# Kernel optimization log

Measured on AMD Instinct MI355X. Metric: run time of the kernel, lower is better.

Reference implementation:

```python
import jax, jax.numpy as jnp
import numpy as np

WINDOW = (2, 7, 7)
SHIFT = (1, 3, 3)
HEADS = 4


def _rel_pos_index(ws):
    coords = np.stack(np.meshgrid(*[np.arange(w) for w in ws], indexing='ij'))  # (3, wd, wh, ww)
    cf = coords.reshape(3, -1)
    rel = cf[:, :, None] - cf[:, None, :]  # (3, N, N)
    rel = rel.transpose(1, 2, 0).astype(np.int64)
    rel[:, :, 0] += ws[0] - 1
    rel[:, :, 1] += ws[1] - 1
    rel[:, :, 2] += ws[2] - 1
    rel[:, :, 0] *= (2 * ws[1] - 1) * (2 * ws[2] - 1)
    rel[:, :, 1] *= 2 * ws[2] - 1
    return rel.sum(-1)  # (N, N)


def _attn_mask(D, H, W, ws, ss):
    img = np.zeros((1, D, H, W, 1), np.float32)
    cnt = 0
    for d in (slice(None, -ws[0]), slice(-ws[0], -ss[0]), slice(-ss[0], None)):
        for h in (slice(None, -ws[1]), slice(-ws[1], -ss[1]), slice(-ss[1], None)):
            for w in (slice(None, -ws[2]), slice(-ws[2], -ss[2]), slice(-ss[2], None)):
                img[:, d, h, w, :] = cnt
                cnt += 1
    N = ws[0] * ws[1] * ws[2]
    mw = img.reshape(1, D // ws[0], ws[0], H // ws[1], ws[1], W // ws[2], ws[2], 1)
    mw = mw.transpose(0, 1, 3, 5, 2, 4, 6, 7).reshape(-1, N)  # (nW, N)
    diff = mw[:, None, :] - mw[:, :, None]
    return np.where(diff != 0, -100.0, 0.0).astype(np.float32)  # (nW, N, N)


def _win_partition(x, ws):
    B, D, H, W, C = x.shape
    x = x.reshape(B, D // ws[0], ws[0], H // ws[1], ws[1], W // ws[2], ws[2], C)
    return x.transpose(0, 1, 3, 5, 2, 4, 6, 7).reshape(-1, ws[0] * ws[1] * ws[2], C)


def _win_reverse(win, ws, B, D, H, W):
    C = win.shape[-1]
    x = win.reshape(B, D // ws[0], H // ws[1], W // ws[2], ws[0], ws[1], ws[2], C)
    return x.transpose(0, 1, 4, 2, 5, 3, 6, 7).reshape(B, D, H, W, C)


def _ln(x, w, b):
    mu = x.mean(-1, keepdims=True)
    var = x.var(-1, keepdims=True)
    return (x - mu) / jnp.sqrt(var + 1e-5) * w + b


def setup_inputs() -> dict:
    key = jax.random.key(0)
    ks = jax.random.split(key, 8)
    B, D, H, W, C = 4, 8, 56, 56, 128
    hidden = 4 * C
    table = (2 * WINDOW[0] - 1) * (2 * WINDOW[1] - 1) * (2 * WINDOW[2] - 1)
    return {
        'x': jax.random.normal(ks[0], (B, D, H, W, C), jnp.float32),
        'norm1_w': jnp.ones((C,), jnp.float32),
        'norm1_b': jnp.zeros((C,), jnp.float32),
        'qkv_w': 0.02 * jax.random.normal(ks[1], (3 * C, C), jnp.float32),
        'qkv_b': jnp.zeros((3 * C,), jnp.float32),
        'rpb': 0.02 * jax.random.normal(ks[2], (table, HEADS), jnp.float32),
        'proj_w': 0.02 * jax.random.normal(ks[3], (C, C), jnp.float32),
        'proj_b': jnp.zeros((C,), jnp.float32),
        'norm2_w': jnp.ones((C,), jnp.float32),
        'norm2_b': jnp.zeros((C,), jnp.float32),
        'fc1_w': 0.02 * jax.random.normal(ks[4], (hidden, C), jnp.float32),
        'fc1_b': jnp.zeros((hidden,), jnp.float32),
        'fc2_w': 0.02 * jax.random.normal(ks[5], (C, hidden), jnp.float32),
        'fc2_b': jnp.zeros((C,), jnp.float32),
    }


def reference(x, norm1_w, norm1_b, qkv_w, qkv_b, rpb, proj_w, proj_b,
              norm2_w, norm2_b, fc1_w, fc1_b, fc2_w, fc2_b):
    B, D, H, W, C = x.shape
    hd = C // HEADS
    scale = hd ** -0.5
    N = WINDOW[0] * WINDOW[1] * WINDOW[2]

    shortcut = x
    y = _ln(x, norm1_w, norm1_b)
    # cyclic shift (SW-MSA)
    y = jnp.roll(y, (-SHIFT[0], -SHIFT[1], -SHIFT[2]), axis=(1, 2, 3))
    win = _win_partition(y, WINDOW)  # (B_, N, C)
    B_ = win.shape[0]

    qkv = win @ qkv_w.T + qkv_b  # (B_, N, 3C)
    qkv = qkv.reshape(B_, N, 3, HEADS, hd).transpose(2, 0, 3, 1, 4)
    q, k, v = qkv[0] * scale, qkv[1], qkv[2]  # (B_, h, N, hd)

    attn = jnp.einsum('bhnd,bhmd->bhnm', q, k)  # (B_, h, N, N)
    rpi = _rel_pos_index(WINDOW)
    bias = rpb[rpi.reshape(-1)].reshape(N, N, HEADS).transpose(2, 0, 1)  # (h, N, N)
    attn = attn + bias[None]

    mask = jnp.asarray(_attn_mask(D, H, W, WINDOW, SHIFT))  # (nW, N, N)
    nW = mask.shape[0]
    attn = attn.reshape(B_ // nW, nW, HEADS, N, N) + mask[None, :, None]
    attn = jax.nn.softmax(attn.reshape(B_, HEADS, N, N), axis=-1)

    out = jnp.einsum('bhnm,bhmd->bhnd', attn, v)
    out = out.transpose(0, 2, 1, 3).reshape(B_, N, C)
    out = out @ proj_w.T + proj_b

    y = _win_reverse(out, WINDOW, B, D, H, W)
    y = jnp.roll(y, SHIFT, axis=(1, 2, 3))  # reverse cyclic shift
    x = shortcut + y

    h = _ln(x, norm2_w, norm2_b)
    h = jax.nn.gelu(h @ fc1_w.T + fc1_b, approximate=False)
    h = h @ fc2_w.T + fc2_b
    return x + h
```

## Files before the change

kernel.cpp:

```cpp
#include <hip/hip_runtime.h>
#include <math.h>

typedef short bf16x8 __attribute__((ext_vector_type(8)));
typedef float f32x4 __attribute__((ext_vector_type(4)));
typedef unsigned short u16;

#define DEVFN static __device__ __forceinline__

DEVFN u16 f2bf(float f) {
  union { float f; unsigned u; } v; v.f = f;
  return (u16)((v.u + 0x7FFFu + ((v.u >> 16) & 1u)) >> 16);
}

DEVFN void gload16(const void* g, void* l) {
  __builtin_amdgcn_global_load_lds(
      (const __attribute__((address_space(1))) void*)g,
      (__attribute__((address_space(3))) void*)l, 16, 0, 0);
}

DEVFN float gelu_fast(float x) {
  float e = __expf(-1.702f * x);
  return x * __builtin_amdgcn_rcpf(1.0f + e);
}

#define TT 100352
#define BWIN 1024

__global__ void convert4_kernel(const float* __restrict__ a, const float* __restrict__ b,
                                const float* __restrict__ c, const float* __restrict__ d,
                                u16* __restrict__ oa, u16* __restrict__ ob,
                                u16* __restrict__ oc, u16* __restrict__ od) {
  int i = blockIdx.x * 256 + threadIdx.x;
  const float* s; u16* o; int off;
  if (i < 49152)       { s = a; o = oa; off = i; }
  else if (i < 65536)  { s = b; o = ob; off = i - 49152; }
  else if (i < 131072) { s = c; o = oc; off = i - 65536; }
  else                 { s = d; o = od; off = i - 131072; }
  o[off] = f2bf(s[off]);
}

__global__ void bias_kernel(const float* __restrict__ rpb, float* __restrict__ bias_full) {
  int idx = blockIdx.x * 256 + threadIdx.x;
  if (idx >= 4 * 9604) return;
  int h = idx / 9604, rem = idx % 9604, i = rem / 98, j = rem % 98;
  int di = i / 49, ri = i % 49, hi = ri / 7, wi = ri % 7;
  int dj = j / 49, rj = j % 49, hj = rj / 7, wj = rj % 7;
  int tidx = (di - dj + 1) * 169 + (hi - hj + 6) * 13 + (wi - wj + 6);
  bias_full[idx] = rpb[tidx * 4 + h];
}

template<int SHIFTED>
__global__ __launch_bounds__(256) void ln_kernel(const float* __restrict__ x,
    const float* __restrict__ w, const float* __restrict__ bterm, u16* __restrict__ out)
{
  int gw = blockIdx.x * 4 + (threadIdx.x >> 6);
  int lane = threadIdx.x & 63;
  size_t src;
  if (SHIFTED) {
    int b_ = gw / 98, n = gw % 98;
    int bb = b_ >> 8, widx = b_ & 255;
    int dw = widx >> 6, hw = (widx >> 3) & 7, ww = widx & 7;
    int dd = n / 49, rr = n % 49, hh = rr / 7, wn = rr % 7;
    int d = (dw * 2 + dd + 1) & 7;
    int h = hw * 7 + hh + 3; if (h >= 56) h -= 56;
    int wq = ww * 7 + wn + 3; if (wq >= 56) wq -= 56;
    src = ((size_t)(((bb * 8 + d) * 56 + h) * 56 + wq)) * 128;
  } else {
    src = (size_t)gw * 128;
  }
  float2 v = *(const float2*)(x + src + lane * 2);
  float s = v.x + v.y, q = v.x * v.x + v.y * v.y;
  #pragma unroll
  for (int m = 1; m < 64; m <<= 1) { s += __shfl_xor(s, m, 64); q += __shfl_xor(q, m, 64); }
  float mu = s * (1.0f / 128.0f);
  float var = q * (1.0f / 128.0f) - mu * mu;
  float rstd = rsqrtf(var + 1e-5f);
  int c = lane * 2;
  float y0 = (v.x - mu) * rstd * w[c] + bterm[c];
  float y1 = (v.y - mu) * rstd * w[c + 1] + bterm[c + 1];
  ushort2 o; o.x = f2bf(y0); o.y = f2bf(y1);
  *(ushort2*)(out + (size_t)gw * 128 + c) = o;
}

template<int EPI>
__global__ __launch_bounds__(256) void gemm_kernel(
    const u16* __restrict__ A, const u16* __restrict__ Bw,
    const float* __restrict__ bias, const float* __restrict__ res,
    void* __restrict__ outp, int M, int N, int K)
{
  __shared__ u16 smem[16384];
  u16* As = smem;
  u16* Bs = smem + 8192;
  const int m0 = blockIdx.x * 128, n0 = blockIdx.y * 128;
  const int t = threadIdx.x;
  const int wid = t >> 6, lane = t & 63;
  const int wr = wid >> 1, wc = wid & 1;
  const int l15 = lane & 15, lhi = lane >> 4;
  const int srow = lane >> 3;
  const int sslot = lane & 7;
  const int gcol = ((sslot ^ srow) << 3);
  f32x4 acc[4][4] = {};
  for (int k0 = 0; k0 < K; k0 += 64) {
    #pragma unroll
    for (int it = 0; it < 4; ++it) {
      const int rbase = it * 32 + wid * 8;
      const int row = rbase + srow;
      gload16(A + (size_t)(m0 + row) * K + k0 + gcol, As + rbase * 64);
      gload16(Bw + (size_t)(n0 + row) * K + k0 + gcol, Bs + rbase * 64);
    }
    __syncthreads();
    #pragma unroll
    for (int kk = 0; kk < 64; kk += 32) {
      bf16x8 af[4], bfr[4];
      const int csw = (kk + lhi * 8) ^ ((l15 & 7) << 3);
      #pragma unroll
      for (int mi = 0; mi < 4; ++mi) af[mi] = *(const bf16x8*)(As + (wr * 64 + mi * 16 + l15) * 64 + csw);
      #pragma unroll
      for (int ni = 0; ni < 4; ++ni) bfr[ni] = *(const bf16x8*)(Bs + (wc * 64 + ni * 16 + l15) * 64 + csw);
      #pragma unroll
      for (int mi = 0; mi < 4; ++mi)
        #pragma unroll
        for (int ni = 0; ni < 4; ++ni)
          acc[mi][ni] = __builtin_amdgcn_mfma_f32_16x16x32_bf16(af[mi], bfr[ni], acc[mi][ni], 0, 0, 0);
    }
    __syncthreads();
  }
  if (EPI == 0) {
    const float smul = (n0 == 0) ? 0.17677669529663689f : 1.0f;
    #pragma unroll
    for (int mi = 0; mi < 4; ++mi)
      #pragma unroll
      for (int ni = 0; ni < 4; ++ni) {
        int col = wc * 64 + ni * 16 + l15;
        float bcol = bias[n0 + col];
        #pragma unroll
        for (int r = 0; r < 4; ++r) {
          int row = wr * 64 + mi * 16 + lhi * 4 + r;
          float v = (acc[mi][ni][r] + bcol) * smul;
          smem[row * 128 + (((col >> 3) ^ (row & 7)) << 3) + (col & 7)] = f2bf(v);
        }
      }
    __syncthreads();
    const int rsub = t >> 4, sl = t & 15;
    #pragma unroll
    for (int j = 0; j < 8; ++j) {
      int row = j * 16 + rsub;
      int4 val = *(const int4*)(smem + row * 128 + ((sl ^ (row & 7)) << 3));
      *(int4*)((u16*)outp + (size_t)(m0 + row) * N + n0 + sl * 8) = val;
    }
  } else {
    #pragma unroll
    for (int mi = 0; mi < 4; ++mi)
      #pragma unroll
      for (int r = 0; r < 4; ++r) {
        int row = m0 + wr * 64 + mi * 16 + lhi * 4 + r;
        int b_ = row / 98, n = row % 98;
        int bb = b_ >> 8, widx = b_ & 255;
        int dw = widx >> 6, hw = (widx >> 3) & 7, ww = widx & 7;
        int dd = n / 49, rr = n % 49, hh = rr / 7, wn = rr % 7;
        int d = (dw * 2 + dd + 1) & 7;
        int h = hw * 7 + hh + 3; if (h >= 56) h -= 56;
        int wq = ww * 7 + wn + 3; if (wq >= 56) wq -= 56;
        size_t dbase = ((size_t)(((bb * 8 + d) * 56 + h) * 56 + wq)) * 128;
        #pragma unroll
        for (int ni = 0; ni < 4; ++ni) {
          int col = n0 + wc * 64 + ni * 16 + l15;
          float v = acc[mi][ni][r] + bias[col];
          ((float*)outp)[dbase + col] = res[dbase + col] + v;
        }
      }
  }
}

__global__ __launch_bounds__(256, 2) void mlp_kernel(
    const u16* __restrict__ A, const u16* __restrict__ W1, const float* __restrict__ b1,
    const u16* __restrict__ W2, const float* __restrict__ b2,
    const float* __restrict__ res, float* __restrict__ outp)
{
  __shared__ u16 smem[34816];
  u16* W1c = smem;
  u16* W2c = smem + 8192;
  u16* HsA = smem + 24576;
  float* b1s = (float*)(smem + 33792);
  float* Pk = (float*)smem;
  const int m0 = blockIdx.x * 128;
  const int t = threadIdx.x, wid = t >> 6, lane = t & 63;
  const int l15 = lane & 15, lhi = lane >> 4;
  const int srow4 = lane >> 4, sslot16 = lane & 15;
  const int srow8 = lane >> 3, sslot8 = lane & 7;
  u16* hs = HsA + wid * 2304;

  #pragma unroll
  for (int it = 0; it < 4; ++it) {
    int rb1 = it * 16 + wid * 4, r1 = rb1 + srow4;
    gload16(W1 + (size_t)r1 * 128 + ((sslot16 ^ (r1 & 7)) << 3), W1c + rb1 * 128);
    int rb2 = it * 32 + wid * 8, r2 = rb2 + srow8;
    gload16(W2 + (size_t)r2 * 512 + ((sslot8 ^ (r2 & 7)) << 3), W2c + rb2 * 64);
  }
  if (t < 128) *(f32x4*)(b1s + t * 4) = *(const f32x4*)(b1 + t * 4);
  bf16x8 areg[2][4];
  #pragma unroll
  for (int mi = 0; mi < 2; ++mi)
    #pragma unroll
    for (int kg = 0; kg < 4; ++kg)
      areg[mi][kg] = *(const bf16x8*)(A + (size_t)(m0 + wid * 32 + mi * 16 + l15) * 128 + kg * 32 + lhi * 8);

  f32x4 accO[2][8] = {};
  __syncthreads();
  for (int hc = 0; hc < 8; ++hc) {
    const int cur = (hc & 1) * 8192;
    if (hc < 7) {
      const int nxt = ((hc + 1) & 1) * 8192;
      #pragma unroll
      for (int it = 0; it < 4; ++it) {
        int rb2 = it * 32 + wid * 8, r2 = rb2 + srow8;
        gload16(W2 + (size_t)r2 * 512 + (hc + 1) * 64 + ((sslot8 ^ (r2 & 7)) << 3),
                W2c + nxt + rb2 * 64);
      }
    }
    f32x4 accH[2][4] = {};
    #pragma unroll
    for (int kk = 0; kk < 4; ++kk) {
      bf16x8 bw[4];
      #pragma unroll
      for (int ni = 0; ni < 4; ++ni) {
        int row = ni * 16 + l15;
        bw[ni] = *(const bf16x8*)(W1c + row * 128 + (((kk * 4 + lhi) ^ (row & 7)) << 3));
      }
      #pragma unroll
      for (int mi = 0; mi < 2; ++mi)
        #pragma unroll
        for (int ni = 0; ni < 4; ++ni)
          accH[mi][ni] = __builtin_amdgcn_mfma_f32_16x16x32_bf16(areg[mi][kk], bw[ni], accH[mi][ni], 0, 0, 0);
    }
    #pragma unroll
    for (int mi = 0; mi < 2; ++mi)
      #pragma unroll
      for (int ni = 0; ni < 4; ++ni) {
        float bb = b1s[hc * 64 + ni * 16 + l15];
        #pragma unroll
        for (int r = 0; r < 4; ++r) {
          int tokl = mi * 16 + lhi * 4 + r;
          hs[tokl * 72 + ni * 16 + l15] = f2bf(gelu_fast(accH[mi][ni][r] + bb));
        }
      }
    __syncthreads();
    if (hc < 7) {
      #pragma unroll
      for (int it = 0; it < 4; ++it) {
        int rb1 = it * 16 + wid * 4, r1 = rb1 + srow4;
        gload16(W1 + (size_t)((hc + 1) * 64 + r1) * 128 + ((sslot16 ^ (r1 & 7)) << 3),
                W1c + rb1 * 128);
      }
    }
    #pragma unroll
    for (int kk = 0; kk < 2; ++kk) {
      bf16x8 ah[2], bw2[8];
      #pragma unroll
      for (int mi = 0; mi < 2; ++mi)
        ah[mi] = *(const bf16x8*)(hs + (mi * 16 + l15) * 72 + kk * 32 + lhi * 8);
      #pragma unroll
      for (int ni = 0; ni < 8; ++ni) {
        int row = ni * 16 + l15;
        bw2[ni] = *(const bf16x8*)(W2c + cur + row * 64 + (((kk * 4 + lhi) ^ (row & 7)) << 3));
      }
      #pragma unroll
      for (int mi = 0; mi < 2; ++mi)
        #pragma unroll
        for (int ni = 0; ni < 8; ++ni)
          accO[mi][ni] = __builtin_amdgcn_mfma_f32_16x16x32_bf16(ah[mi], bw2[ni], accO[mi][ni], 0, 0, 0);
    }
    __syncthreads();
  }
  #pragma unroll
  for (int half = 0; half < 2; ++half) {
    if ((wid >> 1) == half) {
      #pragma unroll
      for (int ni = 0; ni < 8; ++ni) {
        int col = ni * 16 + l15;
        float bv = b2[col];
        #pragma unroll
        for (int mi = 0; mi < 2; ++mi)
          #pragma unroll
          for (int r = 0; r < 4; ++r) {
            int tokl = (wid & 1) * 32 + mi * 16 + lhi * 4 + r;
            Pk[tokl * 132 + col] = accO[mi][ni][r] + bv;
          }
      }
    }
    __syncthreads();
    #pragma unroll
    for (int p = 0; p < 8; ++p) {
      int idx = p * 256 + t;
      int row = idx >> 5, c = (idx & 31) * 4;
      size_t gtok = (size_t)(m0 + half * 64 + row);
      f32x4 v = *(const f32x4*)(Pk + row * 132 + c);
      f32x4 rv = *(const f32x4*)(res + gtok * 128 + c);
      *(f32x4*)(outp + gtok * 128 + c) = v + rv;
    }
    __syncthreads();
  }
}

__global__ __launch_bounds__(64) void attn_kernel(
    const u16* __restrict__ qkv, const float* __restrict__ bias_full,
    u16* __restrict__ out_win)
{
  __shared__ u16 vT[32][136];
  __shared__ u16 P[16][136];
  __shared__ signed char rids[112];
  const int bid = blockIdx.x;
  const int w = bid >> 2, h = bid & 3;
  const int lane = threadIdx.x;
  const int l15 = lane & 15, lhi = lane >> 4;
  const int widx = w & 255;
  const int dw = widx >> 6, hw = (widx >> 3) & 7, ww = widx & 7;

  #pragma unroll
  for (int rep = 0; rep < 2; ++rep) {
    int t2 = lane + rep * 64;
    if (t2 < 112) {
      int rv = 0;
      if (t2 < 98) {
        int dd = t2 / 49, rr = t2 % 49, hh = rr / 7, wn = rr % 7;
        int dp = dw * 2 + dd, hp = hw * 7 + hh, wp = ww * 7 + wn;
        int rd = dp < 6 ? 0 : (dp < 7 ? 1 : 2);
        int rh = hp < 49 ? 0 : (hp < 53 ? 1 : 2);
        int rw2 = wp < 49 ? 0 : (wp < 53 ? 1 : 2);
        rv = rd * 9 + rh * 3 + rw2;
      }
      rids[t2] = (signed char)rv;
    }
  }
  for (int f = lane; f < 160; f += 64) {
    int d = f / 5, c = 96 + (f % 5) * 8;
    *(int4*)&vT[d][c] = (int4){0, 0, 0, 0};
  }
  if (lane < 48) {
    int r = lane / 3, c = 112 + (lane % 3) * 8;
    *(int4*)&P[r][c] = (int4){0, 0, 0, 0};
  }
  const size_t base = (size_t)w * 98 * 384;
  for (int f = lane; f < 392; f += 64) {
    int n = f >> 2, c = (f & 3) * 8;
    int4 v = *(const int4*)(qkv + base + (size_t)n * 384 + 256 + h * 32 + c);
    const u16* pv = (const u16*)&v;
    #pragma unroll
    for (int j = 0; j < 8; ++j) vT[c + j][n] = pv[j];
  }
  __syncthreads();

  const float* bh = bias_full + h * 9604;
  const size_t obase = (size_t)w * 98 * 128;
  for (int mt = 0; mt < 7; ++mt) {
    int qn = mt * 16 + l15; if (qn > 97) qn = 97;
    bf16x8 aq = *(const bf16x8*)(qkv + base + (size_t)qn * 384 + h * 32 + lhi * 8);
    f32x4 sf[7];
    #pragma unroll
    for (int nt = 0; nt < 7; ++nt) {
      int kn = nt * 16 + l15; if (kn > 97) kn = 97;
      bf16x8 bk = *(const bf16x8*)(qkv + base + (size_t)kn * 384 + 128 + h * 32 + lhi * 8);
      f32x4 z = {0.f, 0.f, 0.f, 0.f};
      sf[nt] = __builtin_amdgcn_mfma_f32_16x16x32_bf16(aq, bk, z, 0, 0, 0);
    }
    int irow[4], ridr[4];
    #pragma unroll
    for (int r = 0; r < 4; ++r) {
      irow[r] = mt * 16 + lhi * 4 + r;
      ridr[r] = rids[irow[r] > 111 ? 111 : irow[r]];
    }
    float mx[4] = {-1e30f, -1e30f, -1e30f, -1e30f};
    #pragma unroll
    for (int nt = 0; nt < 7; ++nt) {
      int j = nt * 16 + l15;
      int jc = j > 97 ? 97 : j;
      int rj = rids[j];
      #pragma unroll
      for (int r = 0; r < 4; ++r) {
        float s = sf[nt][r];
        int ic = irow[r] > 97 ? 97 : irow[r];
        s += bh[ic * 98 + jc];
        if (ridr[r] != rj) s -= 100.0f;
        if (j > 97) s = -1e30f;
        sf[nt][r] = s;
        mx[r] = fmaxf(mx[r], s);
      }
    }
    #pragma unroll
    for (int m = 1; m < 16; m <<= 1)
      #pragma unroll
      for (int r = 0; r < 4; ++r) mx[r] = fmaxf(mx[r], __shfl_xor(mx[r], m, 64));
    float sm[4] = {0.f, 0.f, 0.f, 0.f};
    #pragma unroll
    for (int nt = 0; nt < 7; ++nt)
      #pragma unroll
      for (int r = 0; r < 4; ++r) {
        float p = __expf(sf[nt][r] - mx[r]);
        sf[nt][r] = p;
        sm[r] += p;
      }
    #pragma unroll
    for (int m = 1; m < 16; m <<= 1)
      #pragma unroll
      for (int r = 0; r < 4; ++r) sm[r] += __shfl_xor(sm[r], m, 64);
    float inv[4];
    #pragma unroll
    for (int r = 0; r < 4; ++r) inv[r] = 1.0f / sm[r];
    __syncthreads();
    #pragma unroll
    for (int nt = 0; nt < 7; ++nt)
      #pragma unroll
      for (int r = 0; r < 4; ++r)
        P[lhi * 4 + r][nt * 16 + l15] = f2bf(sf[nt][r] * inv[r]);
    __syncthreads();
    f32x4 o0 = {}, o1 = {};
    #pragma unroll
    for (int ks = 0; ks < 4; ++ks) {
      bf16x8 ap  = *(const bf16x8*)(&P[l15][ks * 32 + lhi * 8]);
      bf16x8 bv0 = *(const bf16x8*)(&vT[l15][ks * 32 + lhi * 8]);
      bf16x8 bv1 = *(const bf16x8*)(&vT[16 + l15][ks * 32 + lhi * 8]);
      o0 = __builtin_amdgcn_mfma_f32_16x16x32_bf16(ap, bv0, o0, 0, 0, 0);
      o1 = __builtin_amdgcn_mfma_f32_16x16x32_bf16(ap, bv1, o1, 0, 0, 0);
    }
    #pragma unroll
    for (int r = 0; r < 4; ++r) {
      if (irow[r] < 98) {
        size_t orow = obase + (size_t)irow[r] * 128 + h * 32;
        out_win[orow + l15] = f2bf(o0[r]);
        out_win[orow + 16 + l15] = f2bf(o1[r]);
      }
    }
  }
}

extern "C" void kernel_launch(void* const* d_in, const int* in_sizes, int n_in,
                              void* d_out, int out_size, void* d_ws, size_t ws_size,
                              hipStream_t stream)
{
  const float* x      = (const float*)d_in[0];
  const float* n1w    = (const float*)d_in[1];
  const float* n1b    = (const float*)d_in[2];
  const float* qkv_w  = (const float*)d_in[3];
  const float* qkv_b  = (const float*)d_in[4];
  const float* rpb    = (const float*)d_in[5];
  const float* proj_w = (const float*)d_in[6];
  const float* proj_b = (const float*)d_in[7];
  const float* n2w    = (const float*)d_in[8];
  const float* n2b    = (const float*)d_in[9];
  const float* fc1_w  = (const float*)d_in[10];
  const float* fc1_b  = (const float*)d_in[11];
  const float* fc2_w  = (const float*)d_in[12];
  const float* fc2_b  = (const float*)d_in[13];

  char* p = (char*)d_ws;
  size_t off = 0;
  auto alloc = [&](size_t bytes) { void* r = p + off; off = (off + bytes + 255) & ~(size_t)255; return r; };
  u16*   qkvw_b    = (u16*)alloc(49152 * 2);
  u16*   projw_b   = (u16*)alloc(16384 * 2);
  u16*   fc1w_b    = (u16*)alloc(65536 * 2);
  u16*   fc2w_b    = (u16*)alloc(65536 * 2);
  float* bias_full = (float*)alloc(4 * 9604 * 4);
  u16*   y_win     = (u16*)alloc((size_t)TT * 128 * 2);
  float* x2        = (float*)alloc((size_t)TT * 128 * 4);
  u16*   h1        = (u16*)alloc((size_t)TT * 128 * 2);
  u16*   big       = (u16*)alloc((size_t)TT * 384 * 2);
  if (off > ws_size) return;

  convert4_kernel<<<768, 256, 0, stream>>>(qkv_w, proj_w, fc1_w, fc2_w,
                                           qkvw_b, projw_b, fc1w_b, fc2w_b);
  bias_kernel<<<(4 * 9604 + 255) / 256, 256, 0, stream>>>(rpb, bias_full);
  ln_kernel<1><<<TT / 4, 256, 0, stream>>>(x, n1w, n1b, y_win);
  gemm_kernel<0><<<dim3(TT / 128, 3), 256, 0, stream>>>(y_win, qkvw_b, qkv_b, nullptr, big, TT, 384, 128);
  attn_kernel<<<BWIN * 4, 64, 0, stream>>>(big, bias_full, y_win);
  gemm_kernel<1><<<dim3(TT / 128, 1), 256, 0, stream>>>(y_win, projw_b, proj_b, x, x2, TT, 128, 128);
  ln_kernel<0><<<TT / 4, 256, 0, stream>>>(x2, n2w, n2b, h1);
  mlp_kernel<<<TT / 128, 256, 0, stream>>>(h1, fc1w_b, fc1_b, fc2w_b, fc2_b, x2, (float*)d_out);
}
```

Measured before the change: 220.3 us.

## Fuse second LayerNorm into proj GEMM epilogue and stage K in LDS

The projection GEMM epilogue now stages each 64-row half of the tile in shared memory, adds the residual with vectorized stores, computes LayerNorm-2 per row, and writes the bf16 normalized output directly. This removes the separate ln_kernel pass, which re-read x2 from global memory. The attention kernel also preloads the per-head K block into LDS once instead of reloading K rows from global memory for every query tile. The cost is extra LDS use and barriers in the GEMM epilogue, plus a larger attention shared-memory footprint. h1 is written in spatial token order, matching the old unshifted LN output.

```diff
diff --git a/kernel.cpp b/kernel.cpp
--- a/kernel.cpp
+++ b/kernel.cpp
@@ -49,25 +49,19 @@
   bias_full[idx] = rpb[tidx * 4 + h];
 }
 
-template<int SHIFTED>
 __global__ __launch_bounds__(256) void ln_kernel(const float* __restrict__ x,
     const float* __restrict__ w, const float* __restrict__ bterm, u16* __restrict__ out)
 {
   int gw = blockIdx.x * 4 + (threadIdx.x >> 6);
   int lane = threadIdx.x & 63;
-  size_t src;
-  if (SHIFTED) {
-    int b_ = gw / 98, n = gw % 98;
-    int bb = b_ >> 8, widx = b_ & 255;
-    int dw = widx >> 6, hw = (widx >> 3) & 7, ww = widx & 7;
-    int dd = n / 49, rr = n % 49, hh = rr / 7, wn = rr % 7;
-    int d = (dw * 2 + dd + 1) & 7;
-    int h = hw * 7 + hh + 3; if (h >= 56) h -= 56;
-    int wq = ww * 7 + wn + 3; if (wq >= 56) wq -= 56;
-    src = ((size_t)(((bb * 8 + d) * 56 + h) * 56 + wq)) * 128;
-  } else {
-    src = (size_t)gw * 128;
-  }
+  int b_ = gw / 98, n = gw % 98;
+  int bb = b_ >> 8, widx = b_ & 255;
+  int dw = widx >> 6, hw = (widx >> 3) & 7, ww = widx & 7;
+  int dd = n / 49, rr = n % 49, hh = rr / 7, wn = rr % 7;
+  int d = (dw * 2 + dd + 1) & 7;
+  int h = hw * 7 + hh + 3; if (h >= 56) h -= 56;
+  int wq = ww * 7 + wn + 3; if (wq >= 56) wq -= 56;
+  size_t src = ((size_t)(((bb * 8 + d) * 56 + h) * 56 + wq)) * 128;
   float2 v = *(const float2*)(x + src + lane * 2);
   float s = v.x + v.y, q = v.x * v.x + v.y * v.y;
   #pragma unroll
@@ -86,9 +80,11 @@
 __global__ __launch_bounds__(256) void gemm_kernel(
     const u16* __restrict__ A, const u16* __restrict__ Bw,
     const float* __restrict__ bias, const float* __restrict__ res,
-    void* __restrict__ outp, int M, int N, int K)
+    void* __restrict__ outp, const float* __restrict__ n2w,
+    const float* __restrict__ n2b, u16* __restrict__ h1out,
+    int M, int N, int K)
 {
-  __shared__ u16 smem[16384];
+  __shared__ u16 smem[EPI == 1 ? 17664 : 16384];
   u16* As = smem;
   u16* Bs = smem + 8192;
   const int m0 = blockIdx.x * 128, n0 = blockIdx.y * 128;
@@ -149,26 +145,65 @@
       *(int4*)((u16*)outp + (size_t)(m0 + row) * N + n0 + sl * 8) = val;
     }
   } else {
-    #pragma unroll
-    for (int mi = 0; mi < 4; ++mi)
-      #pragma unroll
-      for (int r = 0; r < 4; ++r) {
-        int row = m0 + wr * 64 + mi * 16 + lhi * 4 + r;
-        int b_ = row / 98, n = row % 98;
+    float* Pk = (float*)smem;
+    #pragma unroll
+    for (int half = 0; half < 2; ++half) {
+      if (wr == half) {
+        #pragma unroll
+        for (int ni = 0; ni < 4; ++ni) {
+          int col = wc * 64 + ni * 16 + l15;
+          float bcol = bias[col];
+          #pragma unroll
+          for (int mi = 0; mi < 4; ++mi)
+            #pragma unroll
+            for (int r = 0; r < 4; ++r)
+              Pk[(mi * 16 + lhi * 4 + r) * 138 + col] = acc[mi][ni][r] + bcol;
+        }
+      }
+      __syncthreads();
+      {
+        int rowl = t >> 2, q = t & 3;
+        int grow = m0 + half * 64 + rowl;
+        int b_ = grow / 98, n = grow % 98;
         int bb = b_ >> 8, widx = b_ & 255;
         int dw = widx >> 6, hw = (widx >> 3) & 7, ww = widx & 7;
         int dd = n / 49, rr = n % 49, hh = rr / 7, wn = rr % 7;
         int d = (dw * 2 + dd + 1) & 7;
-        int h = hw * 7 + hh + 3; if (h >= 56) h -= 56;
+        int hq = hw * 7 + hh + 3; if (hq >= 56) hq -= 56;
         int wq = ww * 7 + wn + 3; if (wq >= 56) wq -= 56;
-        size_t dbase = ((size_t)(((bb * 8 + d) * 56 + h) * 56 + wq)) * 128;
-        #pragma unroll
-        for (int ni = 0; ni < 4; ++ni) {
-          int col = n0 + wc * 64 + ni * 16 + l15;
-          float v = acc[mi][ni][r] + bias[col];
-          ((float*)outp)[dbase + col] = res[dbase + col] + v;
+        size_t dbase = ((size_t)(((bb * 8 + d) * 56 + hq) * 56 + wq)) * 128;
+        f32x4 vals[8];
+        float s = 0.f, sq = 0.f;
+        #pragma unroll
+        for (int j = 0; j < 8; ++j) {
+          int col = j * 16 + q * 4;
+          f32x4 pv = *(const f32x4*)(Pk + rowl * 138 + col);
+          f32x4 rv = *(const f32x4*)(res + dbase + col);
+          f32x4 v = pv + rv;
+          vals[j] = v;
+          *(f32x4*)((float*)outp + dbase + col) = v;
+          s += v[0] + v[1] + v[2] + v[3];
+          sq += v[0]*v[0] + v[1]*v[1] + v[2]*v[2] + v[3]*v[3];
         }
-      }
+        s += __shfl_xor(s, 1, 64);  sq += __shfl_xor(sq, 1, 64);
+        s += __shfl_xor(s, 2, 64);  sq += __shfl_xor(sq, 2, 64);
+        float mu = s * (1.0f / 128.0f);
+        float var = sq * (1.0f / 128.0f) - mu * mu;
+        float rstd = rsqrtf(var + 1e-5f);
+        #pragma unroll
+        for (int j = 0; j < 8; ++j) {
+          int col = j * 16 + q * 4;
+          f32x4 wv = *(const f32x4*)(n2w + col);
+          f32x4 bv = *(const f32x4*)(n2b + col);
+          u16 hb[4];
+          #pragma unroll
+          for (int e = 0; e < 4; ++e)
+            hb[e] = f2bf((vals[j][e] - mu) * rstd * wv[e] + bv[e]);
+          *(int2*)(h1out + dbase + col) = *(const int2*)hb;
+        }
+      }
+      __syncthreads();
+    }
   }
 }
 
@@ -306,6 +341,7 @@
     const u16* __restrict__ qkv, const float* __restrict__ bias_full,
     u16* __restrict__ out_win)
 {
+  __shared__ u16 k_lds[112][40];
   __shared__ u16 vT[32][136];
   __shared__ u16 P[16][136];
   __shared__ signed char rids[112];
@@ -341,6 +377,12 @@
     *(int4*)&P[r][c] = (int4){0, 0, 0, 0};
   }
   const size_t base = (size_t)w * 98 * 384;
+  for (int f = lane; f < 448; f += 64) {
+    int n = f >> 2, c = (f & 3) * 8;
+    int4 v = (int4){0, 0, 0, 0};
+    if (n < 98) v = *(const int4*)(qkv + base + (size_t)n * 384 + 128 + h * 32 + c);
+    *(int4*)(&k_lds[n][c]) = v;
+  }
   for (int f = lane; f < 392; f += 64) {
     int n = f >> 2, c = (f & 3) * 8;
     int4 v = *(const int4*)(qkv + base + (size_t)n * 384 + 256 + h * 32 + c);
@@ -358,8 +400,7 @@
     f32x4 sf[7];
     #pragma unroll
     for (int nt = 0; nt < 7; ++nt) {
-      int kn = nt * 16 + l15; if (kn > 97) kn = 97;
-      bf16x8 bk = *(const bf16x8*)(qkv + base + (size_t)kn * 384 + 128 + h * 32 + lhi * 8);
+      bf16x8 bk = *(const bf16x8*)(&k_lds[nt * 16 + l15][lhi * 8]);
       f32x4 z = {0.f, 0.f, 0.f, 0.f};
       sf[nt] = __builtin_amdgcn_mfma_f32_16x16x32_bf16(aq, bk, z, 0, 0, 0);
     }
@@ -469,10 +510,11 @@
   convert4_kernel<<<768, 256, 0, stream>>>(qkv_w, proj_w, fc1_w, fc2_w,
                                            qkvw_b, projw_b, fc1w_b, fc2w_b);
   bias_kernel<<<(4 * 9604 + 255) / 256, 256, 0, stream>>>(rpb, bias_full);
-  ln_kernel<1><<<TT / 4, 256, 0, stream>>>(x, n1w, n1b, y_win);
-  gemm_kernel<0><<<dim3(TT / 128, 3), 256, 0, stream>>>(y_win, qkvw_b, qkv_b, nullptr, big, TT, 384, 128);
+  ln_kernel<<<TT / 4, 256, 0, stream>>>(x, n1w, n1b, y_win);
+  gemm_kernel<0><<<dim3(TT / 128, 3), 256, 0, stream>>>(y_win, qkvw_b, qkv_b, nullptr, big,
+                                                        nullptr, nullptr, nullptr, TT, 384, 128);
   attn_kernel<<<BWIN * 4, 64, 0, stream>>>(big, bias_full, y_win);
-  gemm_kernel<1><<<dim3(TT / 128, 1), 256, 0, stream>>>(y_win, projw_b, proj_b, x, x2, TT, 128, 128);
-  ln_kernel<0><<<TT / 4, 256, 0, stream>>>(x2, n2w, n2b, h1);
+  gemm_kernel<1><<<dim3(TT / 128, 1), 256, 0, stream>>>(y_win, projw_b, proj_b, x, x2,
+                                                        n2w, n2b, h1, TT, 128, 128);
   mlp_kernel<<<TT / 128, 256, 0, stream>>>(h1, fc1w_b, fc1_b, fc2w_b, fc2_b, x2, (float*)d_out);
 }
```

Result: slower. 226.5 us (+2.8%).
